# Kernel optimization log

Measured on AMD Instinct MI355X. Metric: run time of the kernel, lower is better.

The kernel has to match this reference:

```python
import jax, jax.numpy as jnp
import numpy as np

D_MODEL = 1024
N_HEADS = 16
D_K = D_MODEL // N_HEADS


def setup_inputs() -> dict:
    key = jax.random.key(0)
    ks = jax.random.split(key, 9)
    s = 1.0 / np.sqrt(D_MODEL)
    inp = {
        "x": jax.random.normal(ks[0], (4, 2048, D_MODEL), dtype=jnp.float32),
        "wq": jax.random.normal(ks[1], (D_MODEL, D_MODEL), dtype=jnp.float32) * s,
        "bq": jax.random.normal(ks[2], (D_MODEL,), dtype=jnp.float32) * 0.01,
        "wk": jax.random.normal(ks[3], (D_MODEL, D_MODEL), dtype=jnp.float32) * s,
        "bk": jax.random.normal(ks[4], (D_MODEL,), dtype=jnp.float32) * 0.01,
        "wv": jax.random.normal(ks[5], (D_MODEL, D_MODEL), dtype=jnp.float32) * s,
        "bv": jax.random.normal(ks[6], (D_MODEL,), dtype=jnp.float32) * 0.01,
        "wo": jax.random.normal(ks[7], (D_MODEL, D_MODEL), dtype=jnp.float32) * s,
        "bo": jax.random.normal(ks[8], (D_MODEL,), dtype=jnp.float32) * 0.01,
    }
    return inp


def reference(x, wq, bq, wk, bk, wv, bv, wo, bo):
    B, S, _ = x.shape
    # QKV projections (weights stored [in, out] so y = x @ w + b)
    q = (x @ wq + bq).reshape(B, S, N_HEADS, D_K).transpose(0, 2, 1, 3)  # [B,H,S,Dk]
    k = (x @ wk + bk).reshape(B, S, N_HEADS, D_K).transpose(0, 2, 1, 3)
    v = (x @ wv + bv).reshape(B, S, N_HEADS, D_K).transpose(0, 2, 1, 3)
    scale = 1.0 / jnp.sqrt(jnp.asarray(D_K, dtype=x.dtype))
    scores = jnp.einsum("bhqd,bhkd->bhqk", q, k) * scale  # [B,H,S,S]
    attn = jax.nn.softmax(scores, axis=-1)
    out = jnp.einsum("bhqk,bhkd->bhqd", attn, v)  # [B,H,S,Dk]
    out = out.transpose(0, 2, 1, 3).reshape(B, S, D_MODEL)
    return out @ wo + bo
```

## Files before the change

### kernel.cpp

```cpp
#include <hip/hip_runtime.h>

#define D_MODEL 1024
#define NH 16
#define DK 64
#define BB 4
#define SS 2048
#define MROWS (BB*SS)

typedef __attribute__((ext_vector_type(4))) float f32x4;
typedef __attribute__((ext_vector_type(16))) float f32x16;
typedef __attribute__((ext_vector_type(8))) short short8;
typedef __attribute__((ext_vector_type(4))) float float4v;
typedef __attribute__((ext_vector_type(2))) unsigned u32x2;

typedef const __attribute__((address_space(1))) void* gas_t;
typedef __attribute__((address_space(3))) void* las_t;

static __device__ __forceinline__ ushort f2bf(float f) {
  union { float f; unsigned u; } v; v.f = f;
  unsigned r = 0x7fffu + ((v.u >> 16) & 1u);
  return (ushort)((v.u + r) >> 16);
}

__global__ __launch_bounds__(256) void convert_x_k(const float* __restrict__ x,
                                                   ushort* __restrict__ xb) {
  int i = blockIdx.x * 256 + threadIdx.x;
  float4v v = ((const float4v*)x)[i];
  ushort4 o;
  o.x = f2bf(v.x); o.y = f2bf(v.y); o.z = f2bf(v.z); o.w = f2bf(v.w);
  ((ushort4*)xb)[i] = o;
}

__global__ __launch_bounds__(256) void convert_wt_k(const float* __restrict__ w,
                                                    ushort* __restrict__ wt) {
  __shared__ float tile[64][65];
  int bx = blockIdx.x, by = blockIdx.y;
  int tx = threadIdx.x & 63, ty = threadIdx.x >> 6;
#pragma unroll
  for (int i = 0; i < 16; ++i) {
    int r = i * 4 + ty;
    tile[r][tx] = w[(size_t)(by * 64 + r) * D_MODEL + bx * 64 + tx];
  }
  __syncthreads();
#pragma unroll
  for (int i = 0; i < 16; ++i) {
    int r = i * 4 + ty;
    wt[(size_t)(bx * 64 + r) * D_MODEL + by * 64 + tx] = f2bf(tile[tx][r]);
  }
}

__global__ __launch_bounds__(256) void gemm_qkv_k(const ushort* __restrict__ A,
                                                  const ushort* __restrict__ Bt,
                                                  const float* __restrict__ bq,
                                                  const float* __restrict__ bk,
                                                  const float* __restrict__ bv,
                                                  ushort* __restrict__ Qw,
                                                  ushort* __restrict__ Kw,
                                                  ushort* __restrict__ Vw,
                                                  float qscale) {
  const int K = D_MODEL;
  __shared__ __align__(16) ushort As[128 * 32];
  __shared__ __align__(16) ushort Bs[128 * 32];
  const int nbn = 24;
  int bid = blockIdx.x;
  int wg = (bid & 7) * 192 + (bid >> 3);
  int bm = wg / nbn, bn = wg % nbn;
  const int t = threadIdx.x;
  const int l = t & 63;
  const int w = t >> 6;
  const int g = l >> 4, q = l & 15;
  const int wr = w >> 1, wc = w & 1;

  f32x4 acc[4][4];
#pragma unroll
  for (int m = 0; m < 4; ++m)
#pragma unroll
    for (int n = 0; n < 4; ++n) acc[m][n] = f32x4{0.f, 0.f, 0.f, 0.f};

  const ushort* Ab = A + (size_t)bm * 128 * K;
  const ushort* Bb = Bt + (size_t)bn * 128 * K;

  for (int kt = 0; kt < K; kt += 32) {
    __syncthreads();
#pragma unroll
    for (int i = 0; i < 2; ++i) {
      int c = i * 256 + t;
      __builtin_amdgcn_global_load_lds((gas_t)(Ab + (size_t)(c >> 2) * K + kt + (c & 3) * 8),
                                       (las_t)(As + c * 8), 16, 0, 0);
      __builtin_amdgcn_global_load_lds((gas_t)(Bb + (size_t)(c >> 2) * K + kt + (c & 3) * 8),
                                       (las_t)(Bs + c * 8), 16, 0, 0);
    }
    __syncthreads();
    short8 af[4], bf[4];
#pragma unroll
    for (int m = 0; m < 4; ++m)
      af[m] = *(const short8*)(As + (wr * 64 + m * 16 + q) * 32 + g * 8);
#pragma unroll
    for (int n = 0; n < 4; ++n)
      bf[n] = *(const short8*)(Bs + (wc * 64 + n * 16 + q) * 32 + g * 8);
#pragma unroll
    for (int m = 0; m < 4; ++m)
#pragma unroll
      for (int n = 0; n < 4; ++n)
        acc[m][n] = __builtin_amdgcn_mfma_f32_16x16x32_bf16(af[m], bf[n], acc[m][n], 0, 0, 0);
  }

  const int sec = (bn * 128) >> 10;
  const float* bias = sec == 0 ? bq : (sec == 1 ? bk : bv);
  const float scale = sec == 0 ? qscale : 1.0f;
  ushort* dst = sec == 0 ? Qw : Kw;
  const int rbase0 = bm * 128 + wr * 64 + g * 4;
  const int cbase = (bn * 128 + wc * 64 + q) & 1023;
#pragma unroll
  for (int m = 0; m < 4; ++m) {
    int r0 = rbase0 + m * 16;
#pragma unroll
    for (int n = 0; n < 4; ++n) {
      int c = cbase + n * 16;
      float bv_ = bias[c];
      if (sec == 2) {
        ushort4 pk;
        pk.x = f2bf(acc[m][n][0] + bv_);
        pk.y = f2bf(acc[m][n][1] + bv_);
        pk.z = f2bf(acc[m][n][2] + bv_);
        pk.w = f2bf(acc[m][n][3] + bv_);
        size_t off = (((size_t)((r0 >> 11) * NH + (c >> 6))) * DK + (c & 63)) * (size_t)SS + (r0 & (SS - 1));
        *(ushort4*)(Vw + off) = pk;
      } else {
#pragma unroll
        for (int j = 0; j < 4; ++j) {
          int r = r0 + j;
          float v = (acc[m][n][j] + bv_) * scale;
          size_t off = (((size_t)((r >> 11) * NH + (c >> 6))) * SS + (r & (SS - 1))) * DK + (c & 63);
          dst[off] = f2bf(v);
        }
      }
    }
  }
}

__global__ __launch_bounds__(256) void gemm_out_k(const ushort* __restrict__ A,
                                                  const ushort* __restrict__ Bt,
                                                  const float* __restrict__ bias,
                                                  float* __restrict__ outp) {
  const int K = D_MODEL;
  __shared__ __align__(16) ushort As[128 * 32];
  __shared__ __align__(16) ushort Bs[128 * 32];
  const int nbn = 8;
  int bid = blockIdx.x;
  int wg = (bid & 7) * 64 + (bid >> 3);
  int bm = wg / nbn, bn = wg % nbn;
  const int t = threadIdx.x;
  const int l = t & 63;
  const int w = t >> 6;
  const int g = l >> 4, q = l & 15;
  const int wr = w >> 1, wc = w & 1;

  f32x4 acc[4][4];
#pragma unroll
  for (int m = 0; m < 4; ++m)
#pragma unroll
    for (int n = 0; n < 4; ++n) acc[m][n] = f32x4{0.f, 0.f, 0.f, 0.f};

  const ushort* Ab = A + (size_t)bm * 128 * K;
  const ushort* Bb = Bt + (size_t)bn * 128 * K;

  for (int kt = 0; kt < K; kt += 32) {
    __syncthreads();
#pragma unroll
    for (int i = 0; i < 2; ++i) {
      int c = i * 256 + t;
      __builtin_amdgcn_global_load_lds((gas_t)(Ab + (size_t)(c >> 2) * K + kt + (c & 3) * 8),
                                       (las_t)(As + c * 8), 16, 0, 0);
      __builtin_amdgcn_global_load_lds((gas_t)(Bb + (size_t)(c >> 2) * K + kt + (c & 3) * 8),
                                       (las_t)(Bs + c * 8), 16, 0, 0);
    }
    __syncthreads();
    short8 af[4], bf[4];
#pragma unroll
    for (int m = 0; m < 4; ++m)
      af[m] = *(const short8*)(As + (wr * 64 + m * 16 + q) * 32 + g * 8);
#pragma unroll
    for (int n = 0; n < 4; ++n)
      bf[n] = *(const short8*)(Bs + (wc * 64 + n * 16 + q) * 32 + g * 8);
#pragma unroll
    for (int m = 0; m < 4; ++m)
#pragma unroll
      for (int n = 0; n < 4; ++n)
        acc[m][n] = __builtin_amdgcn_mfma_f32_16x16x32_bf16(af[m], bf[n], acc[m][n], 0, 0, 0);
  }

  const int rbase0 = bm * 128 + wr * 64 + g * 4;
  const int cbase = bn * 128 + wc * 64 + q;
#pragma unroll
  for (int m = 0; m < 4; ++m) {
    int r0 = rbase0 + m * 16;
#pragma unroll
    for (int n = 0; n < 4; ++n) {
      int c = cbase + n * 16;
      float bv = bias[c];
#pragma unroll
      for (int j = 0; j < 4; ++j)
        outp[(size_t)(r0 + j) * D_MODEL + c] = acc[m][n][j] + bv;
    }
  }
}

__global__ __launch_bounds__(256, 4) void attn_k(const ushort* __restrict__ Qm,
                                                 const ushort* __restrict__ Km,
                                                 const ushort* __restrict__ Vm,
                                                 ushort* __restrict__ Ob) {
  __shared__ __align__(16) ushort Ks[2][64 * 64];
  __shared__ __align__(16) ushort Vs[2][64 * 64];
  const int bid = blockIdx.x;
  const int logical = (bid & 7) * 128 + (bid >> 3);
  const int bh = logical >> 4;
  const int qblk = logical & 15;
  const int t = threadIdx.x, l = t & 63, w = t >> 6;
  const int q = l & 31, h = l >> 5;
  const int qsw = q & 7;

  const ushort* Qb = Qm + ((size_t)bh * SS + qblk * 128 + w * 32) * DK;
  const ushort* Kb = Km + (size_t)bh * SS * DK;
  const ushort* Vb = Vm + (size_t)bh * DK * SS;

  short8 qf[4];
#pragma unroll
  for (int ks = 0; ks < 4; ++ks)
    qf[ks] = *(const short8*)(Qb + q * DK + ks * 16 + h * 8);

  f32x16 oacc[2];
#pragma unroll
  for (int d = 0; d < 2; ++d)
#pragma unroll
    for (int r = 0; r < 16; ++r) oacc[d][r] = 0.f;
  float lrun = 0.f;

  const int cg = (l & 7) ^ ((l >> 3) & 7);

#define STAGE(B, KT)                                                                        \
  do {                                                                                      \
    _Pragma("unroll") for (int i_ = 0; i_ < 2; ++i_) {                                      \
      int row_ = w * 16 + i_ * 8 + (l >> 3);                                                \
      __builtin_amdgcn_global_load_lds((gas_t)(Kb + (size_t)((KT) + row_) * DK + cg * 8),   \
                                       (las_t)(Ks[B] + (w * 16 + i_ * 8) * 64 + l * 8),     \
                                       16, 0, 0);                                           \
      __builtin_amdgcn_global_load_lds((gas_t)(Vb + (size_t)row_ * SS + (KT) + cg * 8),     \
                                       (las_t)(Vs[B] + (w * 16 + i_ * 8) * 64 + l * 8),     \
                                       16, 0, 0);                                           \
    }                                                                                       \
  } while (0)

  STAGE(0, 0);
  int cur = 0;

  for (int kt = 0; kt < SS; kt += 64) {
    __syncthreads();
    if (kt + 64 < SS) STAGE(cur ^ 1, kt + 64);

    const ushort* Kc = Ks[cur];
    const ushort* Vc = Vs[cur];

    f32x16 sc[2];
#pragma unroll
    for (int n = 0; n < 2; ++n)
#pragma unroll
      for (int r = 0; r < 16; ++r) sc[n][r] = 0.f;

    __builtin_amdgcn_s_setprio(1);
#pragma unroll
    for (int ks = 0; ks < 4; ++ks) {
      int ch = ((ks * 2 + h) ^ qsw) * 8;
      short8 kf0 = *(const short8*)(Kc + q * 64 + ch);
      short8 kf1 = *(const short8*)(Kc + (32 + q) * 64 + ch);
      sc[0] = __builtin_amdgcn_mfma_f32_32x32x16_bf16(kf0, qf[ks], sc[0], 0, 0, 0);
      sc[1] = __builtin_amdgcn_mfma_f32_32x32x16_bf16(kf1, qf[ks], sc[1], 0, 0, 0);
    }
    __builtin_amdgcn_s_setprio(0);

#pragma unroll
    for (int n = 0; n < 2; ++n)
#pragma unroll
      for (int r = 0; r < 16; ++r) sc[n][r] = __builtin_amdgcn_exp2f(sc[n][r]);

    float s8[8];
#pragma unroll
    for (int i = 0; i < 8; ++i)
      s8[i] = (sc[0][i] + sc[0][i + 8]) + (sc[1][i] + sc[1][i + 8]);
#pragma unroll
    for (int i = 0; i < 4; ++i) s8[i] += s8[i + 4];
    lrun += (s8[0] + s8[1]) + (s8[2] + s8[3]);

    short8 pf[4];
#pragma unroll
    for (int n = 0; n < 2; ++n) {
      unsigned wv[8];
#pragma unroll
      for (int Qd = 0; Qd < 4; ++Qd) {
        unsigned w0, w1;
        asm("v_cvt_pk_bf16_f32 %0, %1, %2" : "=v"(w0) : "v"(sc[n][Qd * 4 + 0]), "v"(sc[n][Qd * 4 + 1]));
        asm("v_cvt_pk_bf16_f32 %0, %1, %2" : "=v"(w1) : "v"(sc[n][Qd * 4 + 2]), "v"(sc[n][Qd * 4 + 3]));
        wv[Qd * 2] = w0; wv[Qd * 2 + 1] = w1;
      }
#pragma unroll
      for (int m = 0; m < 2; ++m) {
        u32x2 r0 = __builtin_amdgcn_permlane32_swap(wv[(2 * m) * 2 + 0], wv[(2 * m + 1) * 2 + 0], false, false);
        u32x2 r1 = __builtin_amdgcn_permlane32_swap(wv[(2 * m) * 2 + 1], wv[(2 * m + 1) * 2 + 1], false, false);
        union { unsigned u[4]; short8 s; } fu;
        fu.u[0] = r0[0]; fu.u[1] = r1[0]; fu.u[2] = r0[1]; fu.u[3] = r1[1];
        pf[n * 2 + m] = fu.s;
      }
    }

    __builtin_amdgcn_s_setprio(1);
#pragma unroll
    for (int kvb = 0; kvb < 4; ++kvb) {
      int ch = ((kvb * 2 + h) ^ qsw) * 8;
      short8 vf0 = *(const short8*)(Vc + q * 64 + ch);
      short8 vf1 = *(const short8*)(Vc + (32 + q) * 64 + ch);
      oacc[0] = __builtin_amdgcn_mfma_f32_32x32x16_bf16(vf0, pf[kvb], oacc[0], 0, 0, 0);
      oacc[1] = __builtin_amdgcn_mfma_f32_32x32x16_bf16(vf1, pf[kvb], oacc[1], 0, 0, 0);
    }
    __builtin_amdgcn_s_setprio(0);
    cur ^= 1;
  }
#undef STAGE

  const int b_ = bh >> 4, h_ = bh & 15;
  float lt = lrun;
  lt += __shfl_xor(lt, 32);
  float inv = 1.0f / lt;
  const int srow = qblk * 128 + w * 32 + q;
#pragma unroll
  for (int d = 0; d < 2; ++d)
#pragma unroll
    for (int rq = 0; rq < 4; ++rq) {
      ushort4 pk;
      pk.x = f2bf(oacc[d][rq * 4 + 0] * inv);
      pk.y = f2bf(oacc[d][rq * 4 + 1] * inv);
      pk.z = f2bf(oacc[d][rq * 4 + 2] * inv);
      pk.w = f2bf(oacc[d][rq * 4 + 3] * inv);
      size_t off = ((size_t)b_ * SS + srow) * D_MODEL + h_ * 64 + d * 32 + rq * 8 + h * 4;
      *(ushort4*)(Ob + off) = pk;
    }
}

extern "C" void kernel_launch(void* const* d_in, const int* in_sizes, int n_in,
                              void* d_out, int out_size, void* d_ws, size_t ws_size,
                              hipStream_t stream) {
  (void)in_sizes; (void)n_in; (void)out_size; (void)ws_size;
  const float* x  = (const float*)d_in[0];
  const float* wq = (const float*)d_in[1];
  const float* bq = (const float*)d_in[2];
  const float* wk = (const float*)d_in[3];
  const float* bk = (const float*)d_in[4];
  const float* wv = (const float*)d_in[5];
  const float* bv = (const float*)d_in[6];
  const float* wo = (const float*)d_in[7];
  const float* bo = (const float*)d_in[8];

  char* ws = (char*)d_ws;
  ushort* xb    = (ushort*)(ws);
  ushort* wqkvt = (ushort*)(ws + 16777216);
  ushort* wot   = (ushort*)(ws + 16777216 + 6291456);
  ushort* Qw    = (ushort*)(ws + 16777216 + 6291456 + 2097152);
  ushort* Kw    = (ushort*)(ws + 16777216 + 6291456 + 2097152 + 16777216);
  ushort* Vw    = (ushort*)(ws + 16777216 + 6291456 + 2097152 + 2 * 16777216);
  ushort* Obw   = xb;

  convert_x_k<<<MROWS * D_MODEL / 4 / 256, 256, 0, stream>>>(x, xb);
  convert_wt_k<<<dim3(16, 16), 256, 0, stream>>>(wq, wqkvt);
  convert_wt_k<<<dim3(16, 16), 256, 0, stream>>>(wk, wqkvt + 1024 * 1024);
  convert_wt_k<<<dim3(16, 16), 256, 0, stream>>>(wv, wqkvt + 2 * 1024 * 1024);
  convert_wt_k<<<dim3(16, 16), 256, 0, stream>>>(wo, wot);

  gemm_qkv_k<<<1536, 256, 0, stream>>>(xb, wqkvt, bq, bk, bv, Qw, Kw, Vw,
                                       0.125f * 1.44269504088896f);

  attn_k<<<1024, 256, 0, stream>>>(Qw, Kw, Vw, Obw);

  gemm_out_k<<<512, 256, 0, stream>>>(Obw, wot, bo, (float*)d_out);
}
```

Before: 202.0 us.

## Double-buffer LDS tiles in projection GEMMs and merge weight conversion launches

```diff
diff --git a/kernel.cpp b/kernel.cpp
--- a/kernel.cpp
+++ b/kernel.cpp
@@ -21,6 +21,12 @@
   unsigned r = 0x7fffu + ((v.u >> 16) & 1u);
   return (ushort)((v.u + r) >> 16);
 }
+
+#define VM_WAIT(N)                                              \
+  do {                                                          \
+    asm volatile("s_waitcnt vmcnt(" #N ")" ::: "memory");       \
+    __builtin_amdgcn_sched_barrier(0);                          \
+  } while (0)
 
 __global__ __launch_bounds__(256) void convert_x_k(const float* __restrict__ x,
                                                    ushort* __restrict__ xb) {
@@ -31,9 +37,22 @@
   ((ushort4*)xb)[i] = o;
 }
 
-__global__ __launch_bounds__(256) void convert_wt_k(const float* __restrict__ w,
-                                                    ushort* __restrict__ wt) {
+__global__ __launch_bounds__(256) void convert_wt4_k(const float* __restrict__ w0,
+                                                     const float* __restrict__ w1,
+                                                     const float* __restrict__ w2,
+                                                     const float* __restrict__ w3,
+                                                     ushort* __restrict__ t0,
+                                                     ushort* __restrict__ t1,
+                                                     ushort* __restrict__ t2,
+                                                     ushort* __restrict__ t3) {
   __shared__ float tile[64][65];
+  const float* w; ushort* wt;
+  switch (blockIdx.z) {
+    case 0: w = w0; wt = t0; break;
+    case 1: w = w1; wt = t1; break;
+    case 2: w = w2; wt = t2; break;
+    default: w = w3; wt = t3; break;
+  }
   int bx = blockIdx.x, by = blockIdx.y;
   int tx = threadIdx.x & 63, ty = threadIdx.x >> 6;
 #pragma unroll
@@ -59,8 +78,8 @@
                                                   ushort* __restrict__ Vw,
                                                   float qscale) {
   const int K = D_MODEL;
-  __shared__ __align__(16) ushort As[128 * 32];
-  __shared__ __align__(16) ushort Bs[128 * 32];
+  __shared__ __align__(16) ushort As[2][128 * 32];
+  __shared__ __align__(16) ushort Bs[2][128 * 32];
   const int nbn = 24;
   int bid = blockIdx.x;
   int wg = (bid & 7) * 192 + (bid >> 3);
@@ -80,30 +99,46 @@
   const ushort* Ab = A + (size_t)bm * 128 * K;
   const ushort* Bb = Bt + (size_t)bn * 128 * K;
 
+#define GSTAGE(BUF, KT)                                                                      \
+  do {                                                                                       \
+    _Pragma("unroll") for (int i_ = 0; i_ < 2; ++i_) {                                       \
+      int c_ = i_ * 256 + t;                                                                 \
+      __builtin_amdgcn_global_load_lds((gas_t)(Ab + (size_t)(c_ >> 2) * K + (KT) + (c_ & 3) * 8), \
+                                       (las_t)(As[BUF] + c_ * 8), 16, 0, 0);                 \
+      __builtin_amdgcn_global_load_lds((gas_t)(Bb + (size_t)(c_ >> 2) * K + (KT) + (c_ & 3) * 8), \
+                                       (las_t)(Bs[BUF] + c_ * 8), 16, 0, 0);                 \
+    }                                                                                        \
+  } while (0)
+
+  GSTAGE(0, 0);
+  int cur = 0;
+
   for (int kt = 0; kt < K; kt += 32) {
-    __syncthreads();
-#pragma unroll
-    for (int i = 0; i < 2; ++i) {
-      int c = i * 256 + t;
-      __builtin_amdgcn_global_load_lds((gas_t)(Ab + (size_t)(c >> 2) * K + kt + (c & 3) * 8),
-                                       (las_t)(As + c * 8), 16, 0, 0);
-      __builtin_amdgcn_global_load_lds((gas_t)(Bb + (size_t)(c >> 2) * K + kt + (c & 3) * 8),
-                                       (las_t)(Bs + c * 8), 16, 0, 0);
-    }
-    __syncthreads();
+    if (kt + 32 < K) {
+      GSTAGE(cur ^ 1, kt + 32);
+      VM_WAIT(4);
+    } else {
+      VM_WAIT(0);
+    }
+    __builtin_amdgcn_s_barrier();
+    __builtin_amdgcn_sched_barrier(0);
     short8 af[4], bf[4];
 #pragma unroll
     for (int m = 0; m < 4; ++m)
-      af[m] = *(const short8*)(As + (wr * 64 + m * 16 + q) * 32 + g * 8);
+      af[m] = *(const short8*)(As[cur] + (wr * 64 + m * 16 + q) * 32 + g * 8);
 #pragma unroll
     for (int n = 0; n < 4; ++n)
-      bf[n] = *(const short8*)(Bs + (wc * 64 + n * 16 + q) * 32 + g * 8);
+      bf[n] = *(const short8*)(Bs[cur] + (wc * 64 + n * 16 + q) * 32 + g * 8);
 #pragma unroll
     for (int m = 0; m < 4; ++m)
 #pragma unroll
       for (int n = 0; n < 4; ++n)
         acc[m][n] = __builtin_amdgcn_mfma_f32_16x16x32_bf16(af[m], bf[n], acc[m][n], 0, 0, 0);
-  }
+    __builtin_amdgcn_sched_barrier(0);
+    __builtin_amdgcn_s_barrier();
+    cur ^= 1;
+  }
+#undef GSTAGE
 
   const int sec = (bn * 128) >> 10;
   const float* bias = sec == 0 ? bq : (sec == 1 ? bk : bv);
@@ -144,8 +179,8 @@
                                                   const float* __restrict__ bias,
                                                   float* __restrict__ outp) {
   const int K = D_MODEL;
-  __shared__ __align__(16) ushort As[128 * 32];
-  __shared__ __align__(16) ushort Bs[128 * 32];
+  __shared__ __align__(16) ushort As[2][128 * 32];
+  __shared__ __align__(16) ushort Bs[2][128 * 32];
   const int nbn = 8;
   int bid = blockIdx.x;
   int wg = (bid & 7) * 64 + (bid >> 3);
@@ -165,30 +200,46 @@
   const ushort* Ab = A + (size_t)bm * 128 * K;
   const ushort* Bb = Bt + (size_t)bn * 128 * K;
 
+#define GSTAGE(BUF, KT)                                                                      \
+  do {                                                                                       \
+    _Pragma("unroll") for (int i_ = 0; i_ < 2; ++i_) {                                       \
+      int c_ = i_ * 256 + t;                                                                 \
+      __builtin_amdgcn_global_load_lds((gas_t)(Ab + (size_t)(c_ >> 2) * K + (KT) + (c_ & 3) * 8), \
+                                       (las_t)(As[BUF] + c_ * 8), 16, 0, 0);                 \
+      __builtin_amdgcn_global_load_lds((gas_t)(Bb + (size_t)(c_ >> 2) * K + (KT) + (c_ & 3) * 8), \
+                                       (las_t)(Bs[BUF] + c_ * 8), 16, 0, 0);                 \
+    }                                                                                        \
+  } while (0)
+
+  GSTAGE(0, 0);
+  int cur = 0;
+
   for (int kt = 0; kt < K; kt += 32) {
-    __syncthreads();
-#pragma unroll
-    for (int i = 0; i < 2; ++i) {
-      int c = i * 256 + t;
-      __builtin_amdgcn_global_load_lds((gas_t)(Ab + (size_t)(c >> 2) * K + kt + (c & 3) * 8),
-                                       (las_t)(As + c * 8), 16, 0, 0);
-      __builtin_amdgcn_global_load_lds((gas_t)(Bb + (size_t)(c >> 2) * K + kt + (c & 3) * 8),
-                                       (las_t)(Bs + c * 8), 16, 0, 0);
-    }
-    __syncthreads();
+    if (kt + 32 < K) {
+      GSTAGE(cur ^ 1, kt + 32);
+      VM_WAIT(4);
+    } else {
+      VM_WAIT(0);
+    }
+    __builtin_amdgcn_s_barrier();
+    __builtin_amdgcn_sched_barrier(0);
     short8 af[4], bf[4];
 #pragma unroll
     for (int m = 0; m < 4; ++m)
-      af[m] = *(const short8*)(As + (wr * 64 + m * 16 + q) * 32 + g * 8);
+      af[m] = *(const short8*)(As[cur] + (wr * 64 + m * 16 + q) * 32 + g * 8);
 #pragma unroll
     for (int n = 0; n < 4; ++n)
-      bf[n] = *(const short8*)(Bs + (wc * 64 + n * 16 + q) * 32 + g * 8);
+      bf[n] = *(const short8*)(Bs[cur] + (wc * 64 + n * 16 + q) * 32 + g * 8);
 #pragma unroll
     for (int m = 0; m < 4; ++m)
 #pragma unroll
       for (int n = 0; n < 4; ++n)
         acc[m][n] = __builtin_amdgcn_mfma_f32_16x16x32_bf16(af[m], bf[n], acc[m][n], 0, 0, 0);
-  }
+    __builtin_amdgcn_sched_barrier(0);
+    __builtin_amdgcn_s_barrier();
+    cur ^= 1;
+  }
+#undef GSTAGE
 
   const int rbase0 = bm * 128 + wr * 64 + g * 4;
   const int cbase = bn * 128 + wc * 64 + q;
@@ -369,10 +420,8 @@
   ushort* Obw   = xb;
 
   convert_x_k<<<MROWS * D_MODEL / 4 / 256, 256, 0, stream>>>(x, xb);
-  convert_wt_k<<<dim3(16, 16), 256, 0, stream>>>(wq, wqkvt);
-  convert_wt_k<<<dim3(16, 16), 256, 0, stream>>>(wk, wqkvt + 1024 * 1024);
-  convert_wt_k<<<dim3(16, 16), 256, 0, stream>>>(wv, wqkvt + 2 * 1024 * 1024);
-  convert_wt_k<<<dim3(16, 16), 256, 0, stream>>>(wo, wot);
+  convert_wt4_k<<<dim3(16, 16, 4), 256, 0, stream>>>(
+      wq, wk, wv, wo, wqkvt, wqkvt + 1024 * 1024, wqkvt + 2 * 1024 * 1024, wot);
 
   gemm_qkv_k<<<1536, 256, 0, stream>>>(xb, wqkvt, bq, bk, bv, Qw, Kw, Vw,
                                        0.125f * 1.44269504088896f);
```

After: 197.2 us. 2.4% less time.
